# Performance work log

Hardware: AMD Instinct MI355X
Metric: run time of the kernel (lower is better)

The kernel has to match this reference:

```python
import jax, jax.numpy as jnp
import numpy as np

NEG_INF = -1e9  # mask fill value used by the original layer
LEAKY_SLOPE = 0.2


def setup_inputs() -> dict:
    key = jax.random.key(0)
    k1, k2, k3, k4 = jax.random.split(key, 4)
    B, N, D_in = 8, 1024, 256
    H, head_dim = 8, 32  # output_dim=256, concat_heads=True
    node_features = jax.random.normal(k1, (B, N, D_in), dtype=jnp.float32)
    adjacency = jax.random.randint(k2, (B, N, N), 0, 2, dtype=jnp.int32)
    W = jax.random.normal(k3, (H, D_in, head_dim), dtype=jnp.float32) * (1.0 / np.sqrt(D_in))
    a = jax.random.normal(k4, (H, 2 * head_dim), dtype=jnp.float32) * (1.0 / np.sqrt(2 * head_dim))
    bias = jnp.zeros((H * head_dim,), dtype=jnp.float32)
    return {"node_features": node_features, "adjacency": adjacency, "W": W, "a": a, "bias": bias}


def reference(node_features, adjacency, W, a, bias):
    # node_features: (B,N,D_in); adjacency: (B,N,N) in {0,1}
    H, _, hd = W.shape
    # Per-head linear transform: (B,H,N,head_dim)
    Wh = jnp.einsum('bni,hij->bhnj', node_features, W)
    # a @ concat(h_i, h_j) == a1 @ h_i + a2 @ h_j  (avoids O(N^2*2hd) concat)
    a1, a2 = a[:, :hd], a[:, hd:]
    e_i = jnp.einsum('bhnj,hj->bhn', Wh, a1)  # (B,H,N) source term
    e_j = jnp.einsum('bhnj,hj->bhn', Wh, a2)  # (B,H,N) target term
    scores = e_i[:, :, :, None] + e_j[:, :, None, :]  # (B,H,N,N)
    # LeakyReLU(0.2) exactly as ops.maximum(x, 0.2*x)
    scores = jnp.maximum(scores, LEAKY_SLOPE * scores)
    mask = adjacency.astype(scores.dtype)[:, None, :, :]  # (B,1,N,N)
    masked = scores * mask + (1.0 - mask) * NEG_INF
    attn = jax.nn.softmax(masked, axis=-1)  # (B,H,N,N)
    attended = jnp.einsum('bhij,bhjk->bhik', attn, Wh)  # (B,H,N,hd)
    B, _, N, _ = attended.shape
    # concat heads -> (B,N,H*hd); head order matches the python loop concat
    out = attended.transpose(0, 2, 1, 3).reshape(B, N, H * hd)
    out = out + bias
    return jax.nn.relu(out)
```

## Files before the change

### kernel.cpp

```cpp
#include <hip/hip_runtime.h>

#define GAT_B   8
#define GAT_N   1024
#define GAT_DIN 256
#define GAT_H   8
#define GAT_HD  32
#define GAT_LOG2E 1.4426950408889634f

typedef unsigned short gu16;
typedef unsigned int   gu32;
typedef unsigned long long gu64;
typedef __bf16 bf16x8 __attribute__((ext_vector_type(8)));
typedef __bf16 bf16x4 __attribute__((ext_vector_type(4)));
typedef float  f32x4v __attribute__((ext_vector_type(4)));

#if __has_builtin(__builtin_amdgcn_exp2f)
#define GAT_EXP2(x) __builtin_amdgcn_exp2f(x)
#else
#define GAT_EXP2(x) exp2f(x)
#endif

__device__ __forceinline__ float gb2f(gu16 u) { return __uint_as_float(((gu32)u) << 16); }

__device__ __forceinline__ void gat_detect(const gu16* p, int t, int* sflag) {
    if (t < 64) {
        int e0 = (p[2 * t]     >> 7) & 0xFF;
        int e1 = (p[2 * t + 1] >> 7) & 0xFF;
        unsigned long long m = __ballot((e0 >= 140) || (e1 >= 140));
        if (t == 0) *sflag = (m != 0ULL);
    }
}

__global__ __launch_bounds__(512) void CustomGATLayer_90348932038855_pack(
    const void* __restrict__ Xv, const void* __restrict__ Wv, __bf16* __restrict__ wfg)
{
    __shared__ int sflag;
    const int t = threadIdx.x, h = blockIdx.x;
    gat_detect((const gu16*)Xv, t, &sflag);
    __syncthreads();
    const int fp32 = sflag;

    if (fp32) {
        const float* ws = (const float*)Wv + (size_t)h * 8192;
        #pragma unroll
        for (int q = 0; q < 4; ++q) {
            int idx = q * 2048 + t * 4;
            int i = idx >> 5, k = idx & 31;
            float4 v = *(const float4*)(ws + idx);
            int d = h * 8192 + (((i >> 5) * 32 + k) * 4 + ((i >> 3) & 3)) * 8 + (i & 7);
            wfg[d] = (__bf16)v.x; wfg[d + 32] = (__bf16)v.y;
            wfg[d + 64] = (__bf16)v.z; wfg[d + 96] = (__bf16)v.w;
        }
    } else {
        const gu16* ws = (const gu16*)Wv + (size_t)h * 8192;
        gu16* wo = (gu16*)wfg;
        #pragma unroll
        for (int q = 0; q < 4; ++q) {
            int idx = q * 2048 + t * 4;
            int i = idx >> 5, k = idx & 31;
            ushort4 v = *(const ushort4*)(ws + idx);
            int d = h * 8192 + (((i >> 5) * 32 + k) * 4 + ((i >> 3) & 3)) * 8 + (i & 7);
            wo[d] = v.x; wo[d + 32] = v.y; wo[d + 64] = v.z; wo[d + 96] = v.w;
        }
    }
}

__global__ __launch_bounds__(512) void CustomGATLayer_90348932038855_kernel(
    const void* __restrict__ Xv, const __bf16* __restrict__ wfg, const void* __restrict__ Av,
    const int* __restrict__ adj, gu32* __restrict__ pk32,
    __bf16* __restrict__ whb, float* __restrict__ e1, float* __restrict__ e2)
{
    __shared__ __align__(16) __bf16 Xl[16][264];
    __shared__ int sflag;

    const int t = threadIdx.x;
    const int bt = blockIdx.x;
    const int M0 = bt * 16, b = M0 >> 10, nloc = M0 & 1023;

    const int arow = t >> 5, adw = t & 31;
    const int* aro = adj + ((size_t)(M0 + arow)) * GAT_N + adw * 32;
    const int4 a0 = *(const int4*)(aro);      const int4 a1 = *(const int4*)(aro + 4);
    const int4 a2 = *(const int4*)(aro + 8);  const int4 a3 = *(const int4*)(aro + 12);
    const int4 a4 = *(const int4*)(aro + 16); const int4 a5 = *(const int4*)(aro + 20);
    const int4 a6 = *(const int4*)(aro + 24); const int4 a7 = *(const int4*)(aro + 28);

    gat_detect((const gu16*)Xv, t, &sflag);

    const int srow = t >> 5, scol = (t & 31) * 8;
    __syncthreads();
    const int fp32 = sflag;

    if (fp32) {
        const float* xs = (const float*)Xv + ((size_t)(b * GAT_N + nloc + srow)) * GAT_DIN + scol;
        float4 x0 = *(const float4*)(xs);
        float4 x1 = *(const float4*)(xs + 4);
        bf16x8 xv;
        xv[0] = (__bf16)x0.x; xv[1] = (__bf16)x0.y; xv[2] = (__bf16)x0.z; xv[3] = (__bf16)x0.w;
        xv[4] = (__bf16)x1.x; xv[5] = (__bf16)x1.y; xv[6] = (__bf16)x1.z; xv[7] = (__bf16)x1.w;
        *(bf16x8*)&Xl[srow][scol] = xv;
    } else {
        const gu16* xs = (const gu16*)Xv + ((size_t)(b * GAT_N + nloc + srow)) * GAT_DIN + scol;
        *(bf16x8*)&Xl[srow][scol] = *(const bf16x8*)xs;
    }
    __syncthreads();

    const int h = t >> 6, l = t & 63, g = l >> 4, c = l & 15;
    const __bf16* wf = wfg + h * 8192;

    f32x4v acc0 = {0.f, 0.f, 0.f, 0.f};
    f32x4v acc1 = {0.f, 0.f, 0.f, 0.f};
    #pragma unroll
    for (int kc = 0; kc < 8; ++kc) {
        bf16x8 af = *(const bf16x8*)&Xl[c][kc * 32 + 8 * g];
        bf16x8 b0 = *(const bf16x8*)(wf + ((kc * 32 + c) * 4 + g) * 8);
        bf16x8 b1 = *(const bf16x8*)(wf + ((kc * 32 + c + 16) * 4 + g) * 8);
        acc0 = __builtin_amdgcn_mfma_f32_16x16x32_bf16(af, b0, acc0, 0, 0, 0);
        acc1 = __builtin_amdgcn_mfma_f32_16x16x32_bf16(af, b1, acc1, 0, 0, 0);
    }

    const int nb = nloc + 4 * g;
    const int jcc = nb >> 5, kg = (nb >> 3) & 3, e0 = nb & 7;
    const size_t fb = (((size_t)(b * GAT_H + h) * 32 + jcc) * 4 + kg) * 32;
    bf16x4 v0, v1;
    v0[0] = (__bf16)acc0[0]; v0[1] = (__bf16)acc0[1];
    v0[2] = (__bf16)acc0[2]; v0[3] = (__bf16)acc0[3];
    v1[0] = (__bf16)acc1[0]; v1[1] = (__bf16)acc1[1];
    v1[2] = (__bf16)acc1[2]; v1[3] = (__bf16)acc1[3];
    *(bf16x4*)(whb + (fb + c) * 8 + e0)      = v0;
    *(bf16x4*)(whb + (fb + c + 16) * 8 + e0) = v1;

    float a1c, a1c16, a2c, a2c16;
    if (fp32) {
        const float* ap = (const float*)Av + h * 2 * GAT_HD;
        a1c = ap[c] * GAT_LOG2E;      a1c16 = ap[c + 16] * GAT_LOG2E;
        a2c = ap[32 + c] * GAT_LOG2E; a2c16 = ap[48 + c] * GAT_LOG2E;
    } else {
        const gu16* ap = (const gu16*)Av + h * 2 * GAT_HD;
        a1c = gb2f(ap[c]) * GAT_LOG2E;      a1c16 = gb2f(ap[c + 16]) * GAT_LOG2E;
        a2c = gb2f(ap[32 + c]) * GAT_LOG2E; a2c16 = gb2f(ap[48 + c]) * GAT_LOG2E;
    }
    float p1[4], p2[4];
    #pragma unroll
    for (int q = 0; q < 4; ++q) {
        p1[q] = acc0[q] * a1c + acc1[q] * a1c16;
        p2[q] = acc0[q] * a2c + acc1[q] * a2c16;
        #pragma unroll
        for (int mm = 1; mm <= 8; mm <<= 1) {
            p1[q] += __shfl_xor(p1[q], mm);
            p2[q] += __shfl_xor(p2[q], mm);
        }
    }
    if (c == 0) {
        const size_t eb = (size_t)(b * GAT_H + h) * GAT_N + nb;
        #pragma unroll
        for (int q = 0; q < 4; ++q) { e1[eb + q] = p1[q]; e2[eb + q] = p2[q]; }
    }

    gu32 m = 0;
    m |= (a0.x != 0 ? 1u : 0u)       | (a0.y != 0 ? 2u : 0u)
       | (a0.z != 0 ? 4u : 0u)       | (a0.w != 0 ? 8u : 0u);
    m |= (a1.x != 0 ? 16u : 0u)      | (a1.y != 0 ? 32u : 0u)
       | (a1.z != 0 ? 64u : 0u)      | (a1.w != 0 ? 128u : 0u);
    m |= (a2.x != 0 ? 256u : 0u)     | (a2.y != 0 ? 512u : 0u)
       | (a2.z != 0 ? 1024u : 0u)    | (a2.w != 0 ? 2048u : 0u);
    m |= (a3.x != 0 ? 4096u : 0u)    | (a3.y != 0 ? 8192u : 0u)
       | (a3.z != 0 ? 16384u : 0u)   | (a3.w != 0 ? 32768u : 0u);
    m |= (a4.x != 0 ? 1u << 16 : 0u) | (a4.y != 0 ? 1u << 17 : 0u)
       | (a4.z != 0 ? 1u << 18 : 0u) | (a4.w != 0 ? 1u << 19 : 0u);
    m |= (a5.x != 0 ? 1u << 20 : 0u) | (a5.y != 0 ? 1u << 21 : 0u)
       | (a5.z != 0 ? 1u << 22 : 0u) | (a5.w != 0 ? 1u << 23 : 0u);
    m |= (a6.x != 0 ? 1u << 24 : 0u) | (a6.y != 0 ? 1u << 25 : 0u)
       | (a6.z != 0 ? 1u << 26 : 0u) | (a6.w != 0 ? 1u << 27 : 0u);
    m |= (a7.x != 0 ? 1u << 28 : 0u) | (a7.y != 0 ? 1u << 29 : 0u)
       | (a7.z != 0 ? 1u << 30 : 0u) | (a7.w != 0 ? 1u << 31 : 0u);
    pk32[((size_t)(M0 + arow)) * 32 + adw] = m;
}

__global__ __launch_bounds__(1024, 8) void CustomGATLayer_90348932038855_attn(
    const void* __restrict__ Xv, const gu32* __restrict__ pk32, const void* __restrict__ biasv,
    const __bf16* __restrict__ whb, const float* __restrict__ e1f, const float* __restrict__ e2f,
    float* __restrict__ out)
{
    __shared__ __align__(16) float e2l[GAT_H][1024];
    __shared__ gu32 pkl[16][33];
    __shared__ int sflag;

    const int t = threadIdx.x;
    const int w = t >> 6, l = t & 63, g = l >> 4, c = l & 15;
    const int h = w & 7, jh = w >> 3;
    const int id = blockIdx.x;
    const int b = id & 7, tile = id >> 3;
    const int i0 = tile * 16;

    gat_detect((const gu16*)Xv, t, &sflag);

    if (t < 512) {
        pkl[t >> 5][t & 31] = pk32[((size_t)(b * GAT_N + i0 + (t >> 5))) * 32 + (t & 31)];
    }
    {
        const float* s = e2f + (size_t)(b * GAT_H + h) * GAT_N + jh * 512;
        float* d = &e2l[h][jh * 512];
        #pragma unroll
        for (int q = 0; q < 2; ++q) {
            int off = (q * 64 + l) * 4;
            *(float4*)(d + off) = *(const float4*)(s + off);
        }
    }
    __syncthreads();
    const int fp32 = sflag;

    const float e1r = e1f[(size_t)(b * GAT_H + h) * GAT_N + i0 + c];
    const __bf16* whr = whb + (size_t)(b * GAT_H + h) * (GAT_N * GAT_HD)
                            + jh * 16384 + g * 256 + c * 8;
    const float* e2h = &e2l[h][jh * 512 + 8 * g];
    const gu32* pkr = &pkl[c][jh * 16];

    bf16x8 wA0 = *(const bf16x8*)(whr),        wA1 = *(const bf16x8*)(whr + 128);
    bf16x8 wB0 = *(const bf16x8*)(whr + 1024), wB1 = *(const bf16x8*)(whr + 1152);

    f32x4v acc0 = {0.f, 0.f, 0.f, 0.f};
    f32x4v acc1 = {0.f, 0.f, 0.f, 0.f};
    f32x4v accS = {0.f, 0.f, 0.f, 0.f};
    bf16x8 onesf;
    #pragma unroll
    for (int e = 0; e < 8; ++e) onesf[e] = (__bf16)1.0f;

#define GAT_WCOMP(EV, IDX) {                        \
        float s_ = e1r + (EV);                      \
        s_ = fmaxf(s_, 0.2f * s_);                  \
        s_ = fminf(s_, 86.0f);                      \
        float w_ = GAT_EXP2(s_);                    \
        w_ = (ab & (1u << IDX)) ? w_ : 0.0f;        \
        pf[IDX] = (__bf16)w_; }

    #pragma unroll 2
    for (int jc = 0; jc < 16; ++jc) {
        const bf16x8 w0 = wA0, w1 = wA1;
        wA0 = wB0; wA1 = wB1;
        if (jc < 14) {
            const __bf16* wn = whr + (jc + 2) * 1024;
            wB0 = *(const bf16x8*)wn; wB1 = *(const bf16x8*)(wn + 128);
        }
        const gu32 ab = (pkr[jc] >> (8 * g)) & 0xFFu;
        float4 ea = *(const float4*)(e2h + jc * 32);
        float4 eb = *(const float4*)(e2h + jc * 32 + 4);
        bf16x8 pf;
        GAT_WCOMP(ea.x, 0) GAT_WCOMP(ea.y, 1)
        GAT_WCOMP(ea.z, 2) GAT_WCOMP(ea.w, 3)
        GAT_WCOMP(eb.x, 4) GAT_WCOMP(eb.y, 5)
        GAT_WCOMP(eb.z, 6) GAT_WCOMP(eb.w, 7)
        acc0 = __builtin_amdgcn_mfma_f32_16x16x32_bf16(pf, w0, acc0, 0, 0, 0);
        acc1 = __builtin_amdgcn_mfma_f32_16x16x32_bf16(pf, w1, acc1, 0, 0, 0);
        accS = __builtin_amdgcn_mfma_f32_16x16x32_bf16(pf, onesf, accS, 0, 0, 0);
    }
#undef GAT_WCOMP

    __syncthreads();
    float4* sc = (float4*)e2l;
    const int slot = h * 64 + l;
    if (jh == 1) {
        sc[slot]        = make_float4(acc0[0], acc0[1], acc0[2], acc0[3]);
        sc[512 + slot]  = make_float4(acc1[0], acc1[1], acc1[2], acc1[3]);
        sc[1024 + slot] = make_float4(accS[0], accS[1], accS[2], accS[3]);
    }
    __syncthreads();
    if (jh == 0) {
        float4 q0 = sc[slot], q1 = sc[512 + slot], q2 = sc[1024 + slot];
        acc0[0] += q0.x; acc0[1] += q0.y; acc0[2] += q0.z; acc0[3] += q0.w;
        acc1[0] += q1.x; acc1[1] += q1.y; acc1[2] += q1.z; acc1[3] += q1.w;
        accS[0] += q2.x; accS[1] += q2.y; accS[2] += q2.z; accS[3] += q2.w;

        float bv0, bv1;
        if (fp32) {
            const float* bp = (const float*)biasv + h * GAT_HD;
            bv0 = bp[c]; bv1 = bp[c + 16];
        } else {
            const gu16* bp = (const gu16*)biasv + h * GAT_HD;
            bv0 = gb2f(bp[c]); bv1 = gb2f(bp[c + 16]);
        }

        float* ob = out + (size_t)(b * GAT_N + i0) * (GAT_H * GAT_HD) + h * GAT_HD + c;
        #pragma unroll
        for (int q = 0; q < 4; ++q) {
            float d = accS[q];
            float r = (d > 0.f) ? (1.0f / d) : 0.0f;
            float o0 = fmaxf(acc0[q] * r + bv0, 0.f);
            float o1 = fmaxf(acc1[q] * r + bv1, 0.f);
            ob[(size_t)(4 * g + q) * (GAT_H * GAT_HD)]      = o0;
            ob[(size_t)(4 * g + q) * (GAT_H * GAT_HD) + 16] = o1;
        }
    }
}

extern "C" void kernel_launch(void* const* d_in, const int* in_sizes, int n_in,
                              void* d_out, int out_size, void* d_ws, size_t ws_size,
                              hipStream_t stream) {
    const void* X    = d_in[0];
    const int*  adj  = (const int*)d_in[1];
    const void* Wm   = d_in[2];
    const void* Av   = d_in[3];
    const void* bias = d_in[4];
    float* outp = (float*)d_out;

    __bf16* whb = (__bf16*)d_ws;
    float* e1   = (float*)(whb + (size_t)GAT_B * GAT_H * GAT_N * GAT_HD);
    float* e2   = e1 + (size_t)GAT_B * GAT_H * GAT_N;
    __bf16* wfg = (__bf16*)(e2 + (size_t)GAT_B * GAT_H * GAT_N);
    gu32* pk32  = (gu32*)(wfg + (size_t)GAT_H * GAT_DIN * GAT_HD);

    CustomGATLayer_90348932038855_pack
        <<<dim3(8), 512, 0, stream>>>(X, Wm, wfg);
    CustomGATLayer_90348932038855_kernel
        <<<dim3(512), 512, 0, stream>>>(X, wfg, Av, adj, pk32, whb, e1, e2);
    CustomGATLayer_90348932038855_attn
        <<<dim3((GAT_N / 16) * GAT_B), 1024, 0, stream>>>(
            X, pk32, bias, whb, e1, e2, outp);
}
```

Measured before the change: 122.0 us.

## Deepen Wh prefetch, precompute bias in pack kernel, drop exp clamp

The attention loop now prefetches Wh fragments three chunks ahead instead of two, to hide more global-load latency at the cost of extra registers. The bias dtype conversion moves into the pack kernel, which writes a float bias buffer, so the attention kernel no longer runs the dtype detection ballot. The projection kernel issues its X loads before the adjacency loads. The fminf clamp before exp2 is removed, which saves one op per element but risks inf overflow for large scores.

```diff
diff --git a/kernel.cpp b/kernel.cpp
--- a/kernel.cpp
+++ b/kernel.cpp
@@ -32,13 +32,26 @@
 }
 
 __global__ __launch_bounds__(512) void CustomGATLayer_90348932038855_pack(
-    const void* __restrict__ Xv, const void* __restrict__ Wv, __bf16* __restrict__ wfg)
+    const void* __restrict__ Xv, const void* __restrict__ Wv, const void* __restrict__ biasv,
+    __bf16* __restrict__ wfg, float* __restrict__ biasf)
 {
     __shared__ int sflag;
     const int t = threadIdx.x, h = blockIdx.x;
     gat_detect((const gu16*)Xv, t, &sflag);
     __syncthreads();
     const int fp32 = sflag;
+
+    if (h == 0 && t < 64) {
+        if (fp32) {
+            const float* bp = (const float*)biasv;
+            #pragma unroll
+            for (int q = 0; q < 4; ++q) biasf[t * 4 + q] = bp[t * 4 + q];
+        } else {
+            const gu16* bp = (const gu16*)biasv;
+            #pragma unroll
+            for (int q = 0; q < 4; ++q) biasf[t * 4 + q] = gb2f(bp[t * 4 + q]);
+        }
+    }
 
     if (fp32) {
         const float* ws = (const float*)Wv + (size_t)h * 8192;
@@ -77,6 +90,21 @@
     const int bt = blockIdx.x;
     const int M0 = bt * 16, b = M0 >> 10, nloc = M0 & 1023;
 
+    gat_detect((const gu16*)Xv, t, &sflag);
+    const int srow = t >> 5, scol = (t & 31) * 8;
+    __syncthreads();
+    const int fp32 = sflag;
+
+    float4 x0, x1; bf16x8 xraw;
+    if (fp32) {
+        const float* xs = (const float*)Xv + ((size_t)(b * GAT_N + nloc + srow)) * GAT_DIN + scol;
+        x0 = *(const float4*)(xs);
+        x1 = *(const float4*)(xs + 4);
+    } else {
+        const gu16* xs = (const gu16*)Xv + ((size_t)(b * GAT_N + nloc + srow)) * GAT_DIN + scol;
+        xraw = *(const bf16x8*)xs;
+    }
+
     const int arow = t >> 5, adw = t & 31;
     const int* aro = adj + ((size_t)(M0 + arow)) * GAT_N + adw * 32;
     const int4 a0 = *(const int4*)(aro);      const int4 a1 = *(const int4*)(aro + 4);
@@ -84,23 +112,13 @@
     const int4 a4 = *(const int4*)(aro + 16); const int4 a5 = *(const int4*)(aro + 20);
     const int4 a6 = *(const int4*)(aro + 24); const int4 a7 = *(const int4*)(aro + 28);
 
-    gat_detect((const gu16*)Xv, t, &sflag);
-
-    const int srow = t >> 5, scol = (t & 31) * 8;
-    __syncthreads();
-    const int fp32 = sflag;
-
     if (fp32) {
-        const float* xs = (const float*)Xv + ((size_t)(b * GAT_N + nloc + srow)) * GAT_DIN + scol;
-        float4 x0 = *(const float4*)(xs);
-        float4 x1 = *(const float4*)(xs + 4);
         bf16x8 xv;
         xv[0] = (__bf16)x0.x; xv[1] = (__bf16)x0.y; xv[2] = (__bf16)x0.z; xv[3] = (__bf16)x0.w;
         xv[4] = (__bf16)x1.x; xv[5] = (__bf16)x1.y; xv[6] = (__bf16)x1.z; xv[7] = (__bf16)x1.w;
         *(bf16x8*)&Xl[srow][scol] = xv;
     } else {
-        const gu16* xs = (const gu16*)Xv + ((size_t)(b * GAT_N + nloc + srow)) * GAT_DIN + scol;
-        *(bf16x8*)&Xl[srow][scol] = *(const bf16x8*)xs;
+        *(bf16x8*)&Xl[srow][scol] = xraw;
     }
     __syncthreads();
 
@@ -177,13 +195,12 @@
 }
 
 __global__ __launch_bounds__(1024, 8) void CustomGATLayer_90348932038855_attn(
-    const void* __restrict__ Xv, const gu32* __restrict__ pk32, const void* __restrict__ biasv,
+    const gu32* __restrict__ pk32, const float* __restrict__ biasf,
     const __bf16* __restrict__ whb, const float* __restrict__ e1f, const float* __restrict__ e2f,
     float* __restrict__ out)
 {
     __shared__ __align__(16) float e2l[GAT_H][1024];
     __shared__ gu32 pkl[16][33];
-    __shared__ int sflag;
 
     const int t = threadIdx.x;
     const int w = t >> 6, l = t & 63, g = l >> 4, c = l & 15;
@@ -192,8 +209,6 @@
     const int b = id & 7, tile = id >> 3;
     const int i0 = tile * 16;
 
-    gat_detect((const gu16*)Xv, t, &sflag);
-
     if (t < 512) {
         pkl[t >> 5][t & 31] = pk32[((size_t)(b * GAT_N + i0 + (t >> 5))) * 32 + (t & 31)];
     }
@@ -207,7 +222,6 @@
         }
     }
     __syncthreads();
-    const int fp32 = sflag;
 
     const float e1r = e1f[(size_t)(b * GAT_H + h) * GAT_N + i0 + c];
     const __bf16* whr = whb + (size_t)(b * GAT_H + h) * (GAT_N * GAT_HD)
@@ -217,6 +231,7 @@
 
     bf16x8 wA0 = *(const bf16x8*)(whr),        wA1 = *(const bf16x8*)(whr + 128);
     bf16x8 wB0 = *(const bf16x8*)(whr + 1024), wB1 = *(const bf16x8*)(whr + 1152);
+    bf16x8 wC0 = *(const bf16x8*)(whr + 2048), wC1 = *(const bf16x8*)(whr + 2176);
 
     f32x4v acc0 = {0.f, 0.f, 0.f, 0.f};
     f32x4v acc1 = {0.f, 0.f, 0.f, 0.f};
@@ -228,7 +243,6 @@
 #define GAT_WCOMP(EV, IDX) {                        \
         float s_ = e1r + (EV);                      \
         s_ = fmaxf(s_, 0.2f * s_);                  \
-        s_ = fminf(s_, 86.0f);                      \
         float w_ = GAT_EXP2(s_);                    \
         w_ = (ab & (1u << IDX)) ? w_ : 0.0f;        \
         pf[IDX] = (__bf16)w_; }
@@ -236,10 +250,10 @@
     #pragma unroll 2
     for (int jc = 0; jc < 16; ++jc) {
         const bf16x8 w0 = wA0, w1 = wA1;
-        wA0 = wB0; wA1 = wB1;
-        if (jc < 14) {
-            const __bf16* wn = whr + (jc + 2) * 1024;
-            wB0 = *(const bf16x8*)wn; wB1 = *(const bf16x8*)(wn + 128);
+        wA0 = wB0; wA1 = wB1; wB0 = wC0; wB1 = wC1;
+        if (jc < 13) {
+            const __bf16* wn = whr + (jc + 3) * 1024;
+            wC0 = *(const bf16x8*)wn; wC1 = *(const bf16x8*)(wn + 128);
         }
         const gu32 ab = (pkr[jc] >> (8 * g)) & 0xFFu;
         float4 ea = *(const float4*)(e2h + jc * 32);
@@ -270,14 +284,8 @@
         acc1[0] += q1.x; acc1[1] += q1.y; acc1[2] += q1.z; acc1[3] += q1.w;
         accS[0] += q2.x; accS[1] += q2.y; accS[2] += q2.z; accS[3] += q2.w;
 
-        float bv0, bv1;
-        if (fp32) {
-            const float* bp = (const float*)biasv + h * GAT_HD;
-            bv0 = bp[c]; bv1 = bp[c + 16];
-        } else {
-            const gu16* bp = (const gu16*)biasv + h * GAT_HD;
-            bv0 = gb2f(bp[c]); bv1 = gb2f(bp[c + 16]);
-        }
+        const float bv0 = biasf[h * GAT_HD + c];
+        const float bv1 = biasf[h * GAT_HD + c + 16];
 
         float* ob = out + (size_t)(b * GAT_N + i0) * (GAT_H * GAT_HD) + h * GAT_HD + c;
         #pragma unroll
@@ -307,12 +315,13 @@
     float* e2   = e1 + (size_t)GAT_B * GAT_H * GAT_N;
     __bf16* wfg = (__bf16*)(e2 + (size_t)GAT_B * GAT_H * GAT_N);
     gu32* pk32  = (gu32*)(wfg + (size_t)GAT_H * GAT_DIN * GAT_HD);
+    float* biasf = (float*)(pk32 + (size_t)GAT_B * GAT_N * 32);
 
     CustomGATLayer_90348932038855_pack
-        <<<dim3(8), 512, 0, stream>>>(X, Wm, wfg);
+        <<<dim3(8), 512, 0, stream>>>(X, Wm, bias, wfg, biasf);
     CustomGATLayer_90348932038855_kernel
         <<<dim3(512), 512, 0, stream>>>(X, wfg, Av, adj, pk32, whb, e1, e2);
     CustomGATLayer_90348932038855_attn
         <<<dim3((GAT_N / 16) * GAT_B), 1024, 0, stream>>>(
-            X, pk32, bias, whb, e1, e2, outp);
-}
+            pk32, biasf, whb, e1, e2, outp);
+}
```

After: 124.9 us. 2.4% more time.
